# Kernel tuning notes

Hardware: AMD Instinct MI355X
Metric: run time of the kernel (lower is better)

The kernel has to match this reference:

```python
import jax, jax.numpy as jnp
from jax import lax
import numpy as np

RADIUS = 0.2
NPOINT = 2048
K = 32


def fps(xyz, npoint):
    # Iterative farthest point sampling. xyz: [N,3] -> int32 indices [npoint].
    n = xyz.shape[0]

    def body(carry, _):
        dist, last = carry
        d = jnp.sum((xyz - xyz[last]) ** 2, axis=-1)
        dist = jnp.minimum(dist, d)
        nxt = jnp.argmax(dist).astype(jnp.int32)
        return (dist, nxt), last

    init = (jnp.full((n,), 1e10, xyz.dtype), jnp.asarray(0, jnp.int32))
    _, idxs = lax.scan(body, init, None, length=npoint)
    return idxs  # starts at point 0, matches CUDA farthest_point_sample


def ball_query(radius, k, xyz, new_xyz):
    # xyz: [N,3], new_xyz: [S,3] -> int32 idx [S,k]: first k points within radius,
    # padded with the first found index (0 if none), matching query_ball_point.
    n = xyz.shape[0]
    d2 = jnp.sum((new_xyz[:, None, :] - xyz[None, :, :]) ** 2, axis=-1)  # [S,N]
    within = d2 < radius * radius
    cand = jnp.where(within, jnp.arange(n, dtype=jnp.int32)[None, :], n)
    cand = jnp.sort(cand, axis=-1)[:, :k]
    first = cand[:, :1]
    first = jnp.where(first >= n, 0, first)
    return jnp.where(cand >= n, first, cand)


def _forward(xyz, points, w0, b0, w1, b1, w2, b2):
    fps_idx = jax.vmap(lambda p: fps(p, NPOINT))(xyz)                     # [B,S]
    new_xyz = jnp.take_along_axis(xyz, fps_idx[..., None], axis=1)       # [B,S,3]
    idx = jax.vmap(lambda p, q: ball_query(RADIUS, K, p, q))(xyz, new_xyz)  # [B,S,K]
    grouped_xyz = jax.vmap(lambda p, i: p[i])(xyz, idx) - new_xyz[:, :, None, :]  # [B,S,K,3]
    grouped_pts = jax.vmap(lambda p, i: p[i])(points, idx)               # [B,S,K,C]
    feat = jnp.concatenate([grouped_xyz, grouped_pts], axis=-1)          # [B,S,K,3+C]
    # shared 1x1-conv MLP == per-point linear layers
    for w, b in ((w0, b0), (w1, b1), (w2, b2)):
        feat = jnp.einsum('bskc,cd->bskd', feat, w) + b
    new_points = jnp.max(feat, axis=2)  # max pool over neighborhood, then squeeze
    return new_xyz, new_points, idx


def setup_inputs() -> dict:
    key = jax.random.key(0)
    ks = jax.random.split(key, 8)
    B, N, C = 8, 8192, 32
    xyz = jax.random.uniform(ks[0], (B, N, 3), dtype=jnp.float32)
    points = jax.random.normal(ks[1], (B, N, C), dtype=jnp.float32)
    dims = [3 + C, 64, 64, 128]
    inp = {"xyz": xyz, "points": points}
    for i in range(3):
        inp[f"w{i}"] = jax.random.normal(ks[2 + i], (dims[i], dims[i + 1]), dtype=jnp.float32) * (dims[i] ** -0.5)
        inp[f"b{i}"] = jnp.zeros((dims[i + 1],), dtype=jnp.float32)
    return inp


def reference(xyz, points, w0, b0, w1, b1, w2, b2):
    return _forward(xyz, points, w0, b0, w1, b1, w2, b2)
```

## Files before the change

kernel.cpp:

```cpp
#include <hip/hip_runtime.h>

typedef unsigned long long u64;
typedef unsigned int u32;

#define Bn 8
#define Nn 8192
#define Sn 2048
#define Kn 32
#define CIN 35
#define COUT 128

__global__ __launch_bounds__(128) void fold_kernel(
    const float* __restrict__ w0, const float* __restrict__ b0,
    const float* __restrict__ w1, const float* __restrict__ b1,
    const float* __restrict__ w2, const float* __restrict__ b2,
    float* __restrict__ Wc, float* __restrict__ bc)
{
    __shared__ float W01[35][64];
    __shared__ float bb[64];
    const int t = threadIdx.x;
    for (int o = t; o < 35 * 64; o += 128) {
        int i = o >> 6, j = o & 63;
        float acc = 0.0f;
        for (int c = 0; c < 64; ++c) acc = fmaf(w0[i * 64 + c], w1[c * 64 + j], acc);
        W01[i][j] = acc;
    }
    for (int j = t; j < 64; j += 128) {
        float acc = b1[j];
        for (int c = 0; c < 64; ++c) acc = fmaf(b0[c], w1[c * 64 + j], acc);
        bb[j] = acc;
    }
    __syncthreads();
    for (int o = t; o < 35 * 128; o += 128) {
        int i = o >> 7, j = o & 127;
        float acc = 0.0f;
        for (int c = 0; c < 64; ++c) acc = fmaf(W01[i][c], w2[c * 128 + j], acc);
        Wc[o] = acc;
    }
    for (int j = t; j < 128; j += 128) {
        float acc = b2[j];
        for (int c = 0; c < 64; ++c) acc = fmaf(bb[c], w2[c * 128 + j], acc);
        bc[j] = acc;
    }
}

#define REP16(M) M(0) M(1) M(2) M(3) M(4) M(5) M(6) M(7) \
                 M(8) M(9) M(10) M(11) M(12) M(13) M(14) M(15)

__global__ __launch_bounds__(512, 1) void fps_kernel(
    const float* __restrict__ xyz, float* __restrict__ new_xyz)
{
    extern __shared__ float lds[];
    float* xs = lds;
    float* ys = lds + Nn;
    float* zs = lds + 2 * Nn;
    __shared__ u64 part[2][8];

    const int b = blockIdx.x;
    const int t = threadIdx.x;
    const int lane = t & 63;
    const int wid = t >> 6;
    const float* base = xyz + (size_t)b * (Nn * 3);

#define FPS_DECL(i) float px##i, py##i, pz##i, dist##i;
    REP16(FPS_DECL)
#undef FPS_DECL

#define FPS_INIT(i) { int j = (t * 16 + i);                              \
        px##i = base[j * 3 + 0];                                         \
        py##i = base[j * 3 + 1];                                         \
        pz##i = base[j * 3 + 2];                                         \
        dist##i = 1e10f;                                                 \
        xs[j] = px##i; ys[j] = py##i; zs[j] = pz##i; }
    REP16(FPS_INIT)
#undef FPS_INIT

    float lx = base[0], ly = base[1], lz = base[2];
    if (t == 0) {
        float* o = new_xyz + (size_t)b * Sn * 3;
        o[0] = lx; o[1] = ly; o[2] = lz;
    }
    __syncthreads();

    for (int i = 1; i < Sn; ++i) {
        float best = -1.0f;
        int bp = 0;
#define FPS_STEP(i) {                                              \
        float dx = px##i - lx;                                     \
        float dy = py##i - ly;                                     \
        float dz = pz##i - lz;                                     \
        float d = fmaf(dz, dz, fmaf(dx, dx, __fmul_rn(dy, dy)));   \
        float nd = fminf(dist##i, d);                              \
        dist##i = nd;                                              \
        bool u = nd > best;                                        \
        best = u ? nd : best;                                      \
        bp = u ? i : bp; }
        REP16(FPS_STEP)
#undef FPS_STEP

        u64 key = ((u64)__float_as_uint(best) << 32) |
                  (u64)(0xFFFFFFFFu - (u32)(t * 16 + bp));
#pragma unroll
        for (int off = 1; off < 64; off <<= 1) {
            u64 ok = __shfl_xor(key, off, 64);
            key = ok > key ? ok : key;
        }
        if (lane == 0) part[i & 1][wid] = key;
        __syncthreads();
        u64 kw = part[i & 1][0];
#pragma unroll
        for (int w = 1; w < 8; ++w) {
            u64 kk = part[i & 1][w];
            kw = kk > kw ? kk : kw;
        }
        u32 widx = 0xFFFFFFFFu - (u32)(kw & 0xFFFFFFFFull);
        lx = xs[widx]; ly = ys[widx]; lz = zs[widx];
        if (t == 0) {
            float* o = new_xyz + ((size_t)b * Sn + i) * 3;
            o[0] = lx; o[1] = ly; o[2] = lz;
        }
    }
}

__global__ __launch_bounds__(256) void ballq_kernel(
    const float* __restrict__ xyz, const float* __restrict__ new_xyz,
    int* __restrict__ idx_int, float* __restrict__ out_idx)
{
    const int wlocal = threadIdx.x >> 6;
    const int lane = threadIdx.x & 63;
    const int gw = blockIdx.x * 4 + wlocal;
    const int b = gw >> 11;
    const float* base = xyz + (size_t)b * (Nn * 3);
    const float cx = new_xyz[(size_t)gw * 3 + 0];
    const float cy = new_xyz[(size_t)gw * 3 + 1];
    const float cz = new_xyz[(size_t)gw * 3 + 2];
    __shared__ int buf[4][Kn];
    const float R2 = 0.039999999105930328f;
    int cnt = 0;
    for (int c = 0; c < Nn && cnt < Kn; c += 64) {
        int j = c + lane;
        float dx = base[j * 3 + 0] - cx;
        float dy = base[j * 3 + 1] - cy;
        float dz = base[j * 3 + 2] - cz;
        float d2 = fmaf(dz, dz, fmaf(dx, dx, __fmul_rn(dy, dy)));
        bool in = d2 < R2;
        u64 m = __ballot(in);
        int rank = (int)__popcll(m & ((1ull << lane) - 1ull));
        int pos = cnt + rank;
        if (in && pos < Kn) buf[wlocal][pos] = j;
        cnt += (int)__popcll(m);
    }
    __syncthreads();
    if (lane < Kn) {
        int first = buf[wlocal][0];
        int v = (lane < cnt) ? buf[wlocal][lane] : first;
        idx_int[(size_t)gw * Kn + lane] = v;
        out_idx[(size_t)gw * Kn + lane] = (float)v;
    }
}

__global__ __launch_bounds__(128) void mlp_kernel(
    const float* __restrict__ xyz, const float* __restrict__ points,
    const float* __restrict__ new_xyz, const int* __restrict__ idx_int,
    const float* __restrict__ Wc, const float* __restrict__ bc,
    float* __restrict__ out_np)
{
    const int g = blockIdx.x;
    const int b = g >> 11;
    const int t = threadIdx.x;
    float wcol[CIN];
#pragma unroll
    for (int c = 0; c < CIN; ++c) wcol[c] = Wc[c * COUT + t];
    const int* ip = idx_int + (size_t)g * Kn;
    const float* xb = xyz + (size_t)b * (Nn * 3);
    const float* pb = points + (size_t)b * (Nn * 32);
    float m = -3.4e38f;
    for (int k = 0; k < Kn; ++k) {
        int n = __builtin_amdgcn_readfirstlane(ip[k]);
        const float* xr = xb + n * 3;
        const float* pr = pb + (size_t)n * 32;
        float acc = xr[0] * wcol[0] + xr[1] * wcol[1] + xr[2] * wcol[2];
#pragma unroll
        for (int c = 0; c < 32; ++c) acc = fmaf(pr[c], wcol[3 + c], acc);
        m = fmaxf(m, acc);
    }
    const float cx = new_xyz[(size_t)g * 3 + 0];
    const float cy = new_xyz[(size_t)g * 3 + 1];
    const float cz = new_xyz[(size_t)g * 3 + 2];
    const float corr = cx * wcol[0] + cy * wcol[1] + cz * wcol[2];
    out_np[(size_t)g * COUT + t] = m - corr + bc[t];
}

extern "C" void kernel_launch(void* const* d_in, const int* in_sizes, int n_in,
                              void* d_out, int out_size, void* d_ws, size_t ws_size,
                              hipStream_t stream) {
    const float* xyz    = (const float*)d_in[0];
    const float* points = (const float*)d_in[1];
    const float* w0 = (const float*)d_in[2];
    const float* b0 = (const float*)d_in[3];
    const float* w1 = (const float*)d_in[4];
    const float* b1 = (const float*)d_in[5];
    const float* w2 = (const float*)d_in[6];
    const float* b2 = (const float*)d_in[7];

    float* out = (float*)d_out;
    float* o_newxyz = out;
    float* o_newpts = out + 49152;
    float* o_idx    = out + 49152 + 2097152;

    int*   idx_int = (int*)d_ws;
    float* Wc = (float*)((char*)d_ws + 2097152);
    float* bc = (float*)((char*)d_ws + 2097152 + 17920);

    const int fps_lds = 3 * Nn * 4;
    hipFuncSetAttribute(reinterpret_cast<const void*>(fps_kernel),
                        hipFuncAttributeMaxDynamicSharedMemorySize, fps_lds);

    fold_kernel<<<1, 128, 0, stream>>>(w0, b0, w1, b1, w2, b2, Wc, bc);
    fps_kernel<<<Bn, 512, fps_lds, stream>>>(xyz, o_newxyz);
    ballq_kernel<<<(Bn * Sn) / 4, 256, 0, stream>>>(xyz, o_newxyz, idx_int, o_idx);
    mlp_kernel<<<Bn * Sn, 128, 0, stream>>>(xyz, points, o_newxyz, idx_int, Wc, bc, o_newpts);
}
```

Measured before the change: 1.963 ms.

## Read FPS point coordinates from LDS each step instead of registers

Each thread's point coordinates are no longer held in 48 registers. They are reloaded from LDS on every FPS iteration, using a strided point assignment (p*512+t) so accesses are coalesced and free of bank conflicts. The cross-wave max reduction becomes a tree instead of a serial chain. This lowers register pressure and shortens the reduction's dependency chain, but adds 48 LDS reads per thread on every one of the 2048 serial iterations, which may cost more than the register savings.

```diff
diff --git a/kernel.cpp b/kernel.cpp
--- a/kernel.cpp
+++ b/kernel.cpp
@@ -62,18 +62,16 @@
     const int wid = t >> 6;
     const float* base = xyz + (size_t)b * (Nn * 3);
 
-#define FPS_DECL(i) float px##i, py##i, pz##i, dist##i;
+#define FPS_DECL(i) float dist##i = 1e10f;
     REP16(FPS_DECL)
 #undef FPS_DECL
 
-#define FPS_INIT(i) { int j = (t * 16 + i);                              \
-        px##i = base[j * 3 + 0];                                         \
-        py##i = base[j * 3 + 1];                                         \
-        pz##i = base[j * 3 + 2];                                         \
-        dist##i = 1e10f;                                                 \
-        xs[j] = px##i; ys[j] = py##i; zs[j] = pz##i; }
-    REP16(FPS_INIT)
-#undef FPS_INIT
+    for (int p = 0; p < 16; ++p) {
+        int j = p * 512 + t;
+        xs[j] = base[j * 3 + 0];
+        ys[j] = base[j * 3 + 1];
+        zs[j] = base[j * 3 + 2];
+    }
 
     float lx = base[0], ly = base[1], lz = base[2];
     if (t == 0) {
@@ -86,9 +84,10 @@
         float best = -1.0f;
         int bp = 0;
 #define FPS_STEP(i) {                                              \
-        float dx = px##i - lx;                                     \
-        float dy = py##i - ly;                                     \
-        float dz = pz##i - lz;                                     \
+        int j##i = i * 512 + t;                                    \
+        float dx = xs[j##i] - lx;                                  \
+        float dy = ys[j##i] - ly;                                  \
+        float dz = zs[j##i] - lz;                                  \
         float d = fmaf(dz, dz, fmaf(dx, dx, __fmul_rn(dy, dy)));   \
         float nd = fminf(dist##i, d);                              \
         dist##i = nd;                                              \
@@ -99,7 +98,7 @@
 #undef FPS_STEP
 
         u64 key = ((u64)__float_as_uint(best) << 32) |
-                  (u64)(0xFFFFFFFFu - (u32)(t * 16 + bp));
+                  (u64)(0xFFFFFFFFu - (u32)(bp * 512 + t));
 #pragma unroll
         for (int off = 1; off < 64; off <<= 1) {
             u64 ok = __shfl_xor(key, off, 64);
@@ -107,12 +106,14 @@
         }
         if (lane == 0) part[i & 1][wid] = key;
         __syncthreads();
-        u64 kw = part[i & 1][0];
-#pragma unroll
-        for (int w = 1; w < 8; ++w) {
-            u64 kk = part[i & 1][w];
-            kw = kk > kw ? kk : kw;
-        }
+        u64 k0 = part[i & 1][0], k1 = part[i & 1][1];
+        u64 k2 = part[i & 1][2], k3 = part[i & 1][3];
+        u64 k4 = part[i & 1][4], k5 = part[i & 1][5];
+        u64 k6 = part[i & 1][6], k7 = part[i & 1][7];
+        k0 = k0 > k1 ? k0 : k1;  k2 = k2 > k3 ? k2 : k3;
+        k4 = k4 > k5 ? k4 : k5;  k6 = k6 > k7 ? k6 : k7;
+        k0 = k0 > k2 ? k0 : k2;  k4 = k4 > k6 ? k4 : k6;
+        u64 kw = k0 > k4 ? k0 : k4;
         u32 widx = 0xFFFFFFFFu - (u32)(kw & 0xFFFFFFFFull);
         lx = xs[widx]; ly = ys[widx]; lz = zs[widx];
         if (t == 0) {
```

Measured after the change: 2.567 ms. 30.8% more time.
